# Kernel tuning notes

Measured on AMD Instinct MI355X. Metric: run time of the kernel, lower is better.

Reference implementation:

```python
import jax, jax.numpy as jnp
import numpy as np

B, N, F = 4, 1024, 256
AVG_DEG = 16.0


def setup_inputs() -> dict:
    key = jax.random.key(0)
    k1, k2, k3, k4 = jax.random.split(key, 4)
    u = jax.random.uniform(k1, (B, N, N))
    A = (u < AVG_DEG / N).astype(jnp.float32)
    A = jnp.maximum(A, jnp.swapaxes(A, 1, 2))            # symmetric
    A = A * (1.0 - jnp.eye(N, dtype=jnp.float32))        # no self loops (added in forward)
    x = jax.random.normal(k2, (B, N, F), dtype=jnp.float32)
    pos = jax.random.normal(k3, (B, N, 3), dtype=jnp.float32)
    order = jax.random.uniform(k4, (B, N), dtype=jnp.float32)  # 'random' ordering priorities
    node_mask = jnp.ones((B, N), dtype=bool)
    return {"x": x, "adj": A, "pos": pos, "order": order, "node_mask": node_mask}


def _select(order, excluded, included, node_mask):
    # Greedy frontier-based node selection (K-MIS with stride=2).
    Bn, Nn = order.shape
    ar = jnp.arange(Nn)
    idx0 = jnp.argmin(order, axis=-1).astype(jnp.int32)           # [B]
    available = node_mask
    frontier = ar[None, :] == idx0[:, None]                        # scatter idx0 -> True
    selected = jnp.zeros_like(available)

    def cond(st):
        av, fr, sel, idx = st
        return av.any()

    def body(st):
        av, fr, sel, idx = st
        current = ar[None, :] == idx[:, None]                      # [B,N] one-hot
        sel = sel | current
        exc_row = jnp.take_along_axis(excluded, idx[:, None, None], axis=1)[:, 0]  # excluded[current]
        inc_row = jnp.take_along_axis(included, idx[:, None, None], axis=1)[:, 0]  # included[current]
        av = av & ~current & ~exc_row
        fr = (fr | inc_row | ~fr.any(-1, keepdims=True)) & av      # restart frontier if empty
        mo = jnp.where(fr, order, jnp.inf)
        midx = jnp.argmin(mo, axis=-1).astype(jnp.int32)
        has_fr = fr.any(-1)
        idx = jnp.where(has_fr, midx, idx)
        return (av, fr, sel, idx)

    _, _, selected, _ = jax.lax.while_loop(cond, body, (available, frontier, selected, idx0))
    return selected


def _forward(x, adj, pos, order, node_mask):
    Nn = adj.shape[1]
    eye = jnp.eye(Nn, dtype=adj.dtype)
    adj1 = jnp.where(node_mask[:, :, None], adj + eye, 0.0)        # adj_k[1] = A + I, masked rows
    adj2 = adj1 @ adj                                              # adj_k[2] = (A+I) @ A
    excluded = adj1 != 0                                           # adj_k[stride-1].bool()
    included = adj2 != 0                                           # adj_k[stride].bool()
    selected = _select(jax.lax.stop_gradient(order), excluded, included, node_mask)
    # pad K to N instead of data-dependent num_nodes; mask zeroes the padding
    mask_f, perm = jax.lax.top_k(selected.astype(jnp.float32), Nn)  # [B,K], [B,K]
    adj_kernel = jnp.take_along_axis(adj1, perm[:, None, :], axis=2)  # [B,N,K]
    # add_pool: adj^T @ x, then mask
    x_p = jnp.einsum('bnk,bnf->bkf', adj_kernel, x) * mask_f[..., None]
    # mean_pool for pos: add_pool / column degree
    deg = adj_kernel.sum(axis=1)[..., None]                        # [B,K,1]
    pos_p = jnp.einsum('bnk,bnc->bkc', adj_kernel, pos) / deg * mask_f[..., None]
    # coarsened adjacency: gather cols then rows of adj_k[stride], mask both sides
    a = jnp.take_along_axis(adj2, perm[:, None, :], axis=2)
    a = jnp.take_along_axis(a, perm[:, :, None], axis=1)
    a = a * mask_f[:, None, :] * mask_f[:, :, None]
    return x_p, pos_p, a, mask_f.astype(bool)


def reference(x, adj, pos, order, node_mask):
    return _forward(x, adj, pos, order, node_mask)
```

## Files before the change

kernel.cpp:

```cpp
#include <hip/hip_runtime.h>
#include <hip/hip_bf16.h>

#define BB 4
#define NN 1024
#define FF 256

typedef __hip_bfloat16 bf16;
typedef unsigned long long u64;
typedef unsigned int u32;
typedef unsigned char u8;

__device__ __forceinline__ float b2f(bf16 v) { return __bfloat162float(v); }
__device__ __forceinline__ bf16 f2b(float v) { return __float2bfloat16(v); }

__device__ __forceinline__ float ldf(const void* p, size_t i, int isf32) {
    return isf32 ? ((const float*)p)[i] : b2f(((const bf16*)p)[i]);
}
__device__ __forceinline__ void stf(float* p, size_t i, float v) { p[i] = v; }
__device__ __forceinline__ void stf(bf16* p, size_t i, float v) { p[i] = f2b(v); }

__global__ void probe_kernel(const void* adj, int* flag) {
    const float* p = (const float*)adj;
    int idx = blockIdx.x * 256 + threadIdx.x;
    float v = p[idx];
    int ok = (v == 0.0f) || (v == 1.0f);
    int allok = __syncthreads_and(ok);
    if (threadIdx.x == 0 && !allok) atomicAnd(flag, 0);
}

__global__ __launch_bounds__(512) void sort_kernel(const void* __restrict__ order,
                                                   int* __restrict__ sp2node,
                                                   int* __restrict__ node2sp,
                                                   const int* __restrict__ flag) {
    const int b = blockIdx.x, t = threadIdx.x;
    const int isf32 = (*flag != 0);
    __shared__ u64 keys[NN];
    for (int i = t; i < NN; i += 512) {
        float v = ldf(order, (size_t)b * NN + i, isf32);
        u32 ub = __float_as_uint(v);
        u32 sk = (ub & 0x80000000u) ? ~ub : (ub | 0x80000000u);
        keys[i] = ((u64)sk << 32) | (u32)i;
    }
    __syncthreads();
    for (int k = 2; k <= NN; k <<= 1) {
        for (int j = k >> 1; j > 0; j >>= 1) {
            for (int i = t; i < NN; i += 512) {
                int ixj = i ^ j;
                if (ixj > i) {
                    bool up = (i & k) == 0;
                    u64 a = keys[i], c = keys[ixj];
                    if ((a > c) == up) { keys[i] = c; keys[ixj] = a; }
                }
            }
            __syncthreads();
        }
    }
    for (int i = t; i < NN; i += 512) {
        int n = (int)(keys[i] & 0xFFFFFFFFu);
        sp2node[b * NN + i] = n;
        node2sp[b * NN + n] = i;
    }
}

__global__ void packA_kernel(const void* __restrict__ adj, u64* __restrict__ bitsA,
                             const int* __restrict__ flag) {
    const int r = blockIdx.x, b = blockIdx.y, t = threadIdx.x;
    const int isf32 = (*flag != 0);
    const size_t base = (size_t)b * NN * NN + (size_t)r * NN;
    for (int i = 0; i < 4; i++) {
        int j = i * 256 + t;
        u64 bal = __ballot(ldf(adj, base + j, isf32) != 0.0f);
        if ((t & 63) == 0) bitsA[((size_t)b * NN + r) * 16 + i * 4 + (t >> 6)] = bal;
    }
}

__global__ void inc_pack_kernel(const u64* __restrict__ bitsA,
                                const int* __restrict__ sp2node,
                                const int* __restrict__ node2sp,
                                u32* __restrict__ packed) {
    const int r = blockIdx.x, b = blockIdx.y, t = threadIdx.x;
    __shared__ u64 myrow[16], incw[16];
    __shared__ unsigned short nbr[192];
    __shared__ int s2nT[NN];
    __shared__ int cnt;
    if (t == 0) cnt = 0;
    if (t < 16) myrow[t] = bitsA[((size_t)b * NN + r) * 16 + t];
    __syncthreads();
    for (int i = 0; i < 4; i++) {
        int j = i * 256 + t;
        if ((myrow[j >> 6] >> (j & 63)) & 1) {
            int p = atomicAdd(&cnt, 1);
            if (p < 192) nbr[p] = (unsigned short)j;
        }
        s2nT[(j & 15) * 64 + (j >> 4)] = sp2node[b * NN + j];
    }
    __syncthreads();
    const int c = min(cnt, 192);
    if (t < 16) {
        u64 v = myrow[t];
        for (int n = 0; n < c; n++) v |= bitsA[((size_t)b * NN + nbr[n]) * 16 + t];
        incw[t] = v;
    }
    __syncthreads();
    if (t < 64) {
        const int s = node2sp[b * NN + r];
        u32 e16 = 0, i16 = 0;
        for (int q = 0; q < 16; q++) {
            int jn = s2nT[q * 64 + t];
            u32 eb = (u32)((myrow[jn >> 6] >> (jn & 63)) & 1) | (u32)(jn == r);
            u32 ib = (u32)((incw[jn >> 6] >> (jn & 63)) & 1);
            e16 |= eb << q;
            i16 |= ib << q;
        }
        packed[((size_t)b * NN + s) * 64 + t] = e16 | (i16 << 16);
    }
}

__global__ __launch_bounds__(256) void select_kernel(const u32* __restrict__ packed,
                                                     const int* __restrict__ node2sp,
                                                     int* __restrict__ perm,
                                                     int* __restrict__ kcount,
                                                     int* __restrict__ sink) {
    const int b = blockIdx.x, t = threadIdx.x;
    __shared__ u8 selS[NN];

    const uint4* pp = (const uint4*)(packed + (size_t)b * NN * 64);
    u32 acc = 0;
    for (int i = t; i < NN * 16; i += 256) {
        uint4 v = pp[i];
        acc ^= v.x ^ v.y ^ v.z ^ v.w;
    }
    if (acc == 0xDEADBEEFu && t == 77777) atomicAdd(sink, 1);
    __syncthreads();

    if (t < 64) {
        const int l = t;
        u32 avail = 0xFFFFu, front = (l == 0) ? 1u : 0u, sel = 0u;
        int cur = 0;
        for (int iter = 0; iter < 2 * NN + 8; ++iter) {
            if (__ballot(avail != 0u) == 0ull) break;
            if ((cur >> 4) == l) sel |= 1u << (cur & 15);
            u32 p = packed[((size_t)b * NN + cur) * 64 + l];
            avail &= ~(p & 0xFFFFu);
            front = (front | (p >> 16)) & avail;
            u64 fb = __ballot(front != 0u);
            if (!fb) {
                front = avail;
                fb = __ballot(front != 0u);
            }
            if (fb) {
                int lf = __ffsll(fb) - 1;
                u32 f = __shfl(front, lf);
                cur = lf * 16 + (__ffs(f) - 1);
            }
        }
        for (int q = 0; q < 16; q++) selS[l * 16 + q] = (sel >> q) & 1u;
    }
    __syncthreads();

    if (t < 64) {
        const int l = t;
        u32 nodesel = 0;
        const int* n2s = node2sp + b * NN;
        for (int q = 0; q < 16; q++)
            nodesel |= ((u32)selS[n2s[l * 16 + q]]) << q;

        int cnt_sel = __popc(nodesel);
        int ps = cnt_sel;
        for (int off = 1; off < 64; off <<= 1) {
            int v = __shfl_up(ps, off);
            if (l >= off) ps += v;
        }
        const int K = __shfl(ps, 63);
        int pos = ps - cnt_sel;
        u32 m = nodesel;
        while (m) { int i = __ffs(m) - 1; perm[b * NN + pos++] = l * 16 + i; m &= m - 1; }
        int posu = K + l * 16 - (ps - cnt_sel);
        m = (~nodesel) & 0xFFFFu;
        while (m) { int i = __ffs(m) - 1; perm[b * NN + posu++] = l * 16 + i; m &= m - 1; }
        if (l == 0) kcount[b] = K;
    }
}

template <typename OUT>
__global__ void pool_kernel(const u64* __restrict__ bitsA, const void* __restrict__ x,
                            const void* __restrict__ pos,
                            const int* __restrict__ perm, const int* __restrict__ kcount,
                            OUT* __restrict__ out_x, OUT* __restrict__ out_pos,
                            OUT* __restrict__ out_mask, const int* __restrict__ flag) {
    const int k = blockIdx.x, b = blockIdx.y, t = threadIdx.x;
    const int isf32 = (*flag != 0);
    const int K = kcount[b];
    OUT* ox = out_x + ((size_t)b * NN + k) * FF;
    OUT* op = out_pos + ((size_t)b * NN + k) * 3;
    if (t == 0) stf(out_mask, (size_t)b * NN + k, k < K ? 1.0f : 0.0f);
    if (k >= K) {
        stf(ox, t, 0.0f);
        if (t < 3) stf(op, t, 0.0f);
        return;
    }
    const int r = perm[b * NN + k];
    __shared__ u64 myrow[16];
    __shared__ unsigned short nbr[192];
    __shared__ int cnt;
    if (t == 0) cnt = 0;
    if (t < 16) myrow[t] = bitsA[((size_t)b * NN + r) * 16 + t];
    __syncthreads();
    for (int i = 0; i < 4; i++) {
        int j = i * 256 + t;
        if ((myrow[j >> 6] >> (j & 63)) & 1) {
            int p = atomicAdd(&cnt, 1);
            if (p < 192) nbr[p] = (unsigned short)j;
        }
    }
    __syncthreads();
    const int c = min(cnt, 192);
    const size_t xb = (size_t)b * NN * FF;
    float acc = ldf(x, xb + (size_t)r * FF + t, isf32);
    for (int n = 0; n < c; n++) acc += ldf(x, xb + (size_t)nbr[n] * FF + t, isf32);
    stf(ox, t, acc);
    if (t < 3) {
        const size_t pb = (size_t)b * NN * 3;
        float pa = ldf(pos, pb + r * 3 + t, isf32);
        for (int n = 0; n < c; n++) pa += ldf(pos, pb + nbr[n] * 3 + t, isf32);
        stf(op, t, pa / (float)(c + 1));
    }
}

template <typename OUT>
__global__ void coarse_adj_kernel(const u64* __restrict__ bitsA,
                                  const int* __restrict__ perm, const int* __restrict__ kcount,
                                  OUT* __restrict__ out_a) {
    const int i = blockIdx.x, b = blockIdx.y, t = threadIdx.x;
    const int K = kcount[b];
    OUT* oa = out_a + ((size_t)b * NN + i) * NN;
    if (i >= K) {
        for (int q = 0; q < 4; q++) stf(oa, t + q * 256, 0.0f);
        return;
    }
    __shared__ int p[NN];
    __shared__ u64 myrow[16];
    const int r = perm[b * NN + i];
    if (t < 16) myrow[t] = bitsA[((size_t)b * NN + r) * 16 + t];
    for (int q = 0; q < 4; q++) { int j = t + q * 256; p[j] = perm[b * NN + j]; }
    __syncthreads();
    for (int q = 0; q < 4; q++) {
        int jj = t + q * 256;
        float v = 0.0f;
        if (jj < K) {
            const int pj = p[jj];
            const u64* rj = bitsA + ((size_t)b * NN + pj) * 16;
            int acc = (int)((myrow[pj >> 6] >> (pj & 63)) & 1);
#pragma unroll
            for (int w = 0; w < 16; w++)
                acc += __popcll(myrow[w] & rj[w]);
            v = (float)acc;
        }
        stf(oa, jj, v);
    }
}

extern "C" void kernel_launch(void* const* d_in, const int* in_sizes, int n_in,
                              void* d_out, int out_size, void* d_ws, size_t ws_size,
                              hipStream_t stream) {
    const void* x     = d_in[0];
    const void* adj   = d_in[1];
    const void* pos   = d_in[2];
    const void* order = d_in[3];

    char* ws = (char*)d_ws;
    size_t off = 0;
    u64* bitsA   = (u64*)(ws + off); off += (size_t)BB * NN * 16 * 8;
    u32* packed  = (u32*)(ws + off); off += (size_t)BB * NN * 64 * 4;
    int* sp2node = (int*)(ws + off); off += (size_t)BB * NN * 4;
    int* node2sp = (int*)(ws + off); off += (size_t)BB * NN * 4;
    int* perm    = (int*)(ws + off); off += (size_t)BB * NN * 4;
    int* kcnt    = (int*)(ws + off); off += BB * 4;
    int* flag    = (int*)(ws + off); off += 4;
    int* sink    = (int*)(ws + off);

    bool outf32 = false;
    size_t osz = 0;
    if (hipMemPtrGetInfo(d_out, &osz) == hipSuccess)
        outf32 = (osz >= 4ull * (size_t)out_size);

    probe_kernel<<<256, 256, 0, stream>>>(adj, flag);
    sort_kernel<<<BB, 512, 0, stream>>>(order, sp2node, node2sp, flag);
    packA_kernel<<<dim3(NN, BB), 256, 0, stream>>>(adj, bitsA, flag);
    inc_pack_kernel<<<dim3(NN, BB), 256, 0, stream>>>(bitsA, sp2node, node2sp, packed);
    select_kernel<<<BB, 256, 0, stream>>>(packed, node2sp, perm, kcnt, sink);

    if (outf32) {
        float* out      = (float*)d_out;
        float* out_x    = out;
        float* out_pos  = out_x + (size_t)BB * NN * FF;
        float* out_a    = out_pos + (size_t)BB * NN * 3;
        float* out_mask = out_a + (size_t)BB * NN * NN;
        pool_kernel<float><<<dim3(NN, BB), 256, 0, stream>>>(bitsA, x, pos, perm, kcnt,
                                                             out_x, out_pos, out_mask, flag);
        coarse_adj_kernel<float><<<dim3(NN, BB), 256, 0, stream>>>(bitsA, perm, kcnt, out_a);
    } else {
        bf16* out      = (bf16*)d_out;
        bf16* out_x    = out;
        bf16* out_pos  = out_x + (size_t)BB * NN * FF;
        bf16* out_a    = out_pos + (size_t)BB * NN * 3;
        bf16* out_mask = out_a + (size_t)BB * NN * NN;
        pool_kernel<bf16><<<dim3(NN, BB), 256, 0, stream>>>(bitsA, x, pos, perm, kcnt,
                                                            out_x, out_pos, out_mask, flag);
        coarse_adj_kernel<bf16><<<dim3(NN, BB), 256, 0, stream>>>(bitsA, perm, kcnt, out_a);
    }
}
```

Baseline: 174.9 us.

## Fuse adjacency packing with sort, merge pool and coarse-adj kernels, parallelize OR

```diff
diff --git a/kernel.cpp b/kernel.cpp
--- a/kernel.cpp
+++ b/kernel.cpp
@@ -10,33 +10,29 @@
 typedef unsigned int u32;
 typedef unsigned char u8;
 
-__device__ __forceinline__ float b2f(bf16 v) { return __bfloat162float(v); }
 __device__ __forceinline__ bf16 f2b(float v) { return __float2bfloat16(v); }
-
-__device__ __forceinline__ float ldf(const void* p, size_t i, int isf32) {
-    return isf32 ? ((const float*)p)[i] : b2f(((const bf16*)p)[i]);
-}
 __device__ __forceinline__ void stf(float* p, size_t i, float v) { p[i] = v; }
 __device__ __forceinline__ void stf(bf16* p, size_t i, float v) { p[i] = f2b(v); }
 
-__global__ void probe_kernel(const void* adj, int* flag) {
-    const float* p = (const float*)adj;
-    int idx = blockIdx.x * 256 + threadIdx.x;
-    float v = p[idx];
-    int ok = (v == 0.0f) || (v == 1.0f);
-    int allok = __syncthreads_and(ok);
-    if (threadIdx.x == 0 && !allok) atomicAnd(flag, 0);
-}
-
-__global__ __launch_bounds__(512) void sort_kernel(const void* __restrict__ order,
-                                                   int* __restrict__ sp2node,
-                                                   int* __restrict__ node2sp,
-                                                   const int* __restrict__ flag) {
-    const int b = blockIdx.x, t = threadIdx.x;
-    const int isf32 = (*flag != 0);
+__global__ __launch_bounds__(512) void pack_sort_kernel(const float* __restrict__ adj,
+                                                        const float* __restrict__ order,
+                                                        u64* __restrict__ bitsA,
+                                                        int* __restrict__ sp2node,
+                                                        int* __restrict__ node2sp) {
+    const int b = blockIdx.y, t = threadIdx.x;
     __shared__ u64 keys[NN];
+    if (blockIdx.x < NN) {
+        const int r = blockIdx.x;
+        const size_t base = (size_t)b * NN * NN + (size_t)r * NN;
+        for (int i = 0; i < 2; i++) {
+            int j = i * 512 + t;
+            u64 bal = __ballot(adj[base + j] != 0.0f);
+            if ((t & 63) == 0) bitsA[((size_t)b * NN + r) * 16 + (j >> 6)] = bal;
+        }
+        return;
+    }
     for (int i = t; i < NN; i += 512) {
-        float v = ldf(order, (size_t)b * NN + i, isf32);
+        float v = order[(size_t)b * NN + i];
         u32 ub = __float_as_uint(v);
         u32 sk = (ub & 0x80000000u) ? ~ub : (ub | 0x80000000u);
         keys[i] = ((u64)sk << 32) | (u32)i;
@@ -62,24 +58,13 @@
     }
 }
 
-__global__ void packA_kernel(const void* __restrict__ adj, u64* __restrict__ bitsA,
-                             const int* __restrict__ flag) {
-    const int r = blockIdx.x, b = blockIdx.y, t = threadIdx.x;
-    const int isf32 = (*flag != 0);
-    const size_t base = (size_t)b * NN * NN + (size_t)r * NN;
-    for (int i = 0; i < 4; i++) {
-        int j = i * 256 + t;
-        u64 bal = __ballot(ldf(adj, base + j, isf32) != 0.0f);
-        if ((t & 63) == 0) bitsA[((size_t)b * NN + r) * 16 + i * 4 + (t >> 6)] = bal;
-    }
-}
-
 __global__ void inc_pack_kernel(const u64* __restrict__ bitsA,
                                 const int* __restrict__ sp2node,
                                 const int* __restrict__ node2sp,
                                 u32* __restrict__ packed) {
     const int r = blockIdx.x, b = blockIdx.y, t = threadIdx.x;
     __shared__ u64 myrow[16], incw[16];
+    __shared__ u64 part[256];
     __shared__ unsigned short nbr[192];
     __shared__ int s2nT[NN];
     __shared__ int cnt;
@@ -96,10 +81,18 @@
     }
     __syncthreads();
     const int c = min(cnt, 192);
+    {
+        const int w = t & 15, g = t >> 4;
+        u64 v = 0;
+        for (int n = g; n < c; n += 16)
+            v |= bitsA[((size_t)b * NN + nbr[n]) * 16 + w];
+        part[t] = v;
+    }
+    __syncthreads();
     if (t < 16) {
-        u64 v = myrow[t];
-        for (int n = 0; n < c; n++) v |= bitsA[((size_t)b * NN + nbr[n]) * 16 + t];
-        incw[t] = v;
+        u64 acc = myrow[t];
+        for (int g = 0; g < 16; g++) acc |= part[g * 16 + t];
+        incw[t] = acc;
     }
     __syncthreads();
     if (t < 64) {
@@ -130,7 +123,7 @@
         uint4 v = pp[i];
         acc ^= v.x ^ v.y ^ v.z ^ v.w;
     }
-    if (acc == 0xDEADBEEFu && t == 77777) atomicAdd(sink, 1);
+    if (acc == 0xDEADBEEFu) atomicAdd(sink, 1);
     __syncthreads();
 
     if (t < 64) {
@@ -138,7 +131,6 @@
         u32 avail = 0xFFFFu, front = (l == 0) ? 1u : 0u, sel = 0u;
         int cur = 0;
         for (int iter = 0; iter < 2 * NN + 8; ++iter) {
-            if (__ballot(avail != 0u) == 0ull) break;
             if ((cur >> 4) == l) sel |= 1u << (cur & 15);
             u32 p = packed[((size_t)b * NN + cur) * 64 + l];
             avail &= ~(p & 0xFFFFu);
@@ -147,12 +139,11 @@
             if (!fb) {
                 front = avail;
                 fb = __ballot(front != 0u);
+                if (!fb) break;
             }
-            if (fb) {
-                int lf = __ffsll(fb) - 1;
-                u32 f = __shfl(front, lf);
-                cur = lf * 16 + (__ffs(f) - 1);
-            }
+            int lf = __ffsll(fb) - 1;
+            u32 f = __shfl(front, lf);
+            cur = lf * 16 + (__ffs(f) - 1);
         }
         for (int q = 0; q < 16; q++) selS[l * 16 + q] = (sel >> q) & 1u;
     }
@@ -183,78 +174,64 @@
 }
 
 template <typename OUT>
-__global__ void pool_kernel(const u64* __restrict__ bitsA, const void* __restrict__ x,
-                            const void* __restrict__ pos,
-                            const int* __restrict__ perm, const int* __restrict__ kcount,
-                            OUT* __restrict__ out_x, OUT* __restrict__ out_pos,
-                            OUT* __restrict__ out_mask, const int* __restrict__ flag) {
+__global__ void fused_out_kernel(const u64* __restrict__ bitsA, const float* __restrict__ x,
+                                 const float* __restrict__ pos,
+                                 const int* __restrict__ perm, const int* __restrict__ kcount,
+                                 OUT* __restrict__ out_x, OUT* __restrict__ out_pos,
+                                 OUT* __restrict__ out_a, OUT* __restrict__ out_mask) {
     const int k = blockIdx.x, b = blockIdx.y, t = threadIdx.x;
-    const int isf32 = (*flag != 0);
     const int K = kcount[b];
     OUT* ox = out_x + ((size_t)b * NN + k) * FF;
     OUT* op = out_pos + ((size_t)b * NN + k) * 3;
+    OUT* oa = out_a + ((size_t)b * NN + k) * NN;
     if (t == 0) stf(out_mask, (size_t)b * NN + k, k < K ? 1.0f : 0.0f);
     if (k >= K) {
         stf(ox, t, 0.0f);
         if (t < 3) stf(op, t, 0.0f);
+        for (int q = 0; q < 4; q++) stf(oa, t + q * 256, 0.0f);
         return;
     }
     const int r = perm[b * NN + k];
+    __shared__ int p[NN];
     __shared__ u64 myrow[16];
     __shared__ unsigned short nbr[192];
     __shared__ int cnt;
     if (t == 0) cnt = 0;
     if (t < 16) myrow[t] = bitsA[((size_t)b * NN + r) * 16 + t];
+    for (int q = 0; q < 4; q++) { int j = t + q * 256; p[j] = perm[b * NN + j]; }
     __syncthreads();
     for (int i = 0; i < 4; i++) {
         int j = i * 256 + t;
         if ((myrow[j >> 6] >> (j & 63)) & 1) {
-            int p = atomicAdd(&cnt, 1);
-            if (p < 192) nbr[p] = (unsigned short)j;
+            int pp = atomicAdd(&cnt, 1);
+            if (pp < 192) nbr[pp] = (unsigned short)j;
         }
     }
     __syncthreads();
     const int c = min(cnt, 192);
+
     const size_t xb = (size_t)b * NN * FF;
-    float acc = ldf(x, xb + (size_t)r * FF + t, isf32);
-    for (int n = 0; n < c; n++) acc += ldf(x, xb + (size_t)nbr[n] * FF + t, isf32);
+    float acc = x[xb + (size_t)r * FF + t];
+    for (int n = 0; n < c; n++) acc += x[xb + (size_t)nbr[n] * FF + t];
     stf(ox, t, acc);
     if (t < 3) {
         const size_t pb = (size_t)b * NN * 3;
-        float pa = ldf(pos, pb + r * 3 + t, isf32);
-        for (int n = 0; n < c; n++) pa += ldf(pos, pb + nbr[n] * 3 + t, isf32);
+        float pa = pos[pb + r * 3 + t];
+        for (int n = 0; n < c; n++) pa += pos[pb + nbr[n] * 3 + t];
         stf(op, t, pa / (float)(c + 1));
     }
-}
-
-template <typename OUT>
-__global__ void coarse_adj_kernel(const u64* __restrict__ bitsA,
-                                  const int* __restrict__ perm, const int* __restrict__ kcount,
-                                  OUT* __restrict__ out_a) {
-    const int i = blockIdx.x, b = blockIdx.y, t = threadIdx.x;
-    const int K = kcount[b];
-    OUT* oa = out_a + ((size_t)b * NN + i) * NN;
-    if (i >= K) {
-        for (int q = 0; q < 4; q++) stf(oa, t + q * 256, 0.0f);
-        return;
-    }
-    __shared__ int p[NN];
-    __shared__ u64 myrow[16];
-    const int r = perm[b * NN + i];
-    if (t < 16) myrow[t] = bitsA[((size_t)b * NN + r) * 16 + t];
-    for (int q = 0; q < 4; q++) { int j = t + q * 256; p[j] = perm[b * NN + j]; }
-    __syncthreads();
+
     for (int q = 0; q < 4; q++) {
         int jj = t + q * 256;
         float v = 0.0f;
         if (jj < K) {
             const int pj = p[jj];
             const u64* rj = bitsA + ((size_t)b * NN + pj) * 16;
-            int acc = (int)((myrow[pj >> 6] >> (pj & 63)) & 1);
+            int a2 = (int)((myrow[pj >> 6] >> (pj & 63)) & 1);
 #pragma unroll
             for (int w = 0; w < 16; w++)
-                acc += __popcll(myrow[w] & rj[w]);
-            v = (float)acc;
+                a2 += __popcll(myrow[w] & rj[w]);
+            v = (float)a2;
         }
         stf(oa, jj, v);
     }
@@ -263,10 +240,10 @@
 extern "C" void kernel_launch(void* const* d_in, const int* in_sizes, int n_in,
                               void* d_out, int out_size, void* d_ws, size_t ws_size,
                               hipStream_t stream) {
-    const void* x     = d_in[0];
-    const void* adj   = d_in[1];
-    const void* pos   = d_in[2];
-    const void* order = d_in[3];
+    const float* x     = (const float*)d_in[0];
+    const float* adj   = (const float*)d_in[1];
+    const float* pos   = (const float*)d_in[2];
+    const float* order = (const float*)d_in[3];
 
     char* ws = (char*)d_ws;
     size_t off = 0;
@@ -276,7 +253,6 @@
     int* node2sp = (int*)(ws + off); off += (size_t)BB * NN * 4;
     int* perm    = (int*)(ws + off); off += (size_t)BB * NN * 4;
     int* kcnt    = (int*)(ws + off); off += BB * 4;
-    int* flag    = (int*)(ws + off); off += 4;
     int* sink    = (int*)(ws + off);
 
     bool outf32 = false;
@@ -284,9 +260,7 @@
     if (hipMemPtrGetInfo(d_out, &osz) == hipSuccess)
         outf32 = (osz >= 4ull * (size_t)out_size);
 
-    probe_kernel<<<256, 256, 0, stream>>>(adj, flag);
-    sort_kernel<<<BB, 512, 0, stream>>>(order, sp2node, node2sp, flag);
-    packA_kernel<<<dim3(NN, BB), 256, 0, stream>>>(adj, bitsA, flag);
+    pack_sort_kernel<<<dim3(NN + 1, BB), 512, 0, stream>>>(adj, order, bitsA, sp2node, node2sp);
     inc_pack_kernel<<<dim3(NN, BB), 256, 0, stream>>>(bitsA, sp2node, node2sp, packed);
     select_kernel<<<BB, 256, 0, stream>>>(packed, node2sp, perm, kcnt, sink);
 
@@ -296,17 +270,15 @@
         float* out_pos  = out_x + (size_t)BB * NN * FF;
         float* out_a    = out_pos + (size_t)BB * NN * 3;
         float* out_mask = out_a + (size_t)BB * NN * NN;
-        pool_kernel<float><<<dim3(NN, BB), 256, 0, stream>>>(bitsA, x, pos, perm, kcnt,
-                                                             out_x, out_pos, out_mask, flag);
-        coarse_adj_kernel<float><<<dim3(NN, BB), 256, 0, stream>>>(bitsA, perm, kcnt, out_a);
+        fused_out_kernel<float><<<dim3(NN, BB), 256, 0, stream>>>(bitsA, x, pos, perm, kcnt,
+                                                                  out_x, out_pos, out_a, out_mask);
     } else {
         bf16* out      = (bf16*)d_out;
         bf16* out_x    = out;
         bf16* out_pos  = out_x + (size_t)BB * NN * FF;
         bf16* out_a    = out_pos + (size_t)BB * NN * 3;
         bf16* out_mask = out_a + (size_t)BB * NN * NN;
-        pool_kernel<bf16><<<dim3(NN, BB), 256, 0, stream>>>(bitsA, x, pos, perm, kcnt,
-                                                            out_x, out_pos, out_mask, flag);
-        coarse_adj_kernel<bf16><<<dim3(NN, BB), 256, 0, stream>>>(bitsA, perm, kcnt, out_a);
-    }
-}
+        fused_out_kernel<bf16><<<dim3(NN, BB), 256, 0, stream>>>(bitsA, x, pos, perm, kcnt,
+                                                                 out_x, out_pos, out_a, out_mask);
+    }
+}
```

Result: faster. 151.7 us (-13.2%).
